# Kernel optimization log

Measured on AMD Instinct MI355X. Metric: run time of the kernel, lower is better.

The kernel has to match this reference:

```python
import jax, jax.numpy as jnp
import numpy as np

CLAMP = 10.0  # forward default arg `clamp`


def setup_inputs() -> dict:
    key = jax.random.key(0)
    k1, k2, k3, k4 = jax.random.split(key, 4)
    B, N = 256, 8192
    return {
        "pred_frames": jax.random.normal(k1, (B, N, 4, 4), dtype=jnp.float32),
        "true_frames": jax.random.normal(k2, (B, N, 4, 4), dtype=jnp.float32),
        "pred_pos": jax.random.normal(k3, (B, N, 3), dtype=jnp.float32),
        "true_pos": jax.random.normal(k4, (B, N, 3), dtype=jnp.float32),
    }


def reference(pred_frames, true_frames, pred_pos, true_pos):
    # Batched Kabsch alignment of pred_pos -> true_pos, then clamped point error.
    # pred_frames / true_frames are unused by the original module's forward.
    cA = pred_pos.mean(axis=1, keepdims=True)  # [B,1,3]
    cB = true_pos.mean(axis=1, keepdims=True)  # [B,1,3]
    AA = pred_pos - cA                          # [B,N,3]
    BB = true_pos - cB                          # [B,N,3]
    H = jnp.einsum('bni,bnj->bij', AA, BB)      # [B,3,3] covariance
    U, S, Vt = jnp.linalg.svd(H)
    # R = Vt^T @ U^T : R[b,i,k] = sum_j Vt[b,j,i] * U[b,k,j]
    R = jnp.einsum('bji,bkj->bik', Vt, U)
    det = jnp.linalg.det(R)                     # [B]
    sign = jnp.where(det < 0, -1.0, 1.0).astype(Vt.dtype)
    Vt_fixed = Vt.at[:, -1, :].multiply(sign[:, None])  # flip last row if det<0
    R = jnp.einsum('bji,bkj->bik', Vt_fixed, U)
    # t = centroid_B - R @ centroid_A (vector of shape [B,3])
    t = cB[:, 0, :] - jnp.einsum('bij,bj->bi', R, cA[:, 0, :])
    # NOTE: original applies pred_pos @ R (not R^T) + t, replicated faithfully.
    pred_aligned = jnp.einsum('bni,bij->bnj', pred_pos, R) + t[:, None, :]
    dist = jnp.linalg.norm(pred_aligned - true_pos, axis=-1)  # [B,N]
    # clamp(max=CLAMP).mean() per batch, then averaged over batch == global mean
    return jnp.mean(jnp.minimum(dist, CLAMP))
```

## Files before the change

### kernel.cpp

```cpp
#include <hip/hip_runtime.h>
#include <math.h>

#define NB 256
#define NPT 8192
#define SPLITS 4
#define CHUNK (NPT / SPLITS)
#define THREADS 256
#define CLAMPV 10.0f
#define INV_TOTAL (1.0f / 2097152.0f)

__global__ __launch_bounds__(THREADS) void cov_kernel(
    const float* __restrict__ pred, const float* __restrict__ tru,
    float* __restrict__ stats)
{
    const int blk = blockIdx.x;
    const int b  = blk >> 2;
    const int sp = blk & 3;
    const float* P = pred + ((size_t)b * NPT + (size_t)sp * CHUNK) * 3;
    const float* T = tru  + ((size_t)b * NPT + (size_t)sp * CHUNK) * 3;

    float acc[15];
#pragma unroll
    for (int i = 0; i < 15; ++i) acc[i] = 0.f;

    for (int n0 = threadIdx.x * 4; n0 < CHUNK; n0 += THREADS * 4) {
        const float4* Pq = (const float4*)(P + 3 * n0);
        const float4* Tq = (const float4*)(T + 3 * n0);
        const float4 pa = Pq[0], pb = Pq[1], pc = Pq[2];
        const float4 ta = Tq[0], tb = Tq[1], tc = Tq[2];
        const float px[4] = {pa.x, pa.w, pb.z, pc.y};
        const float py[4] = {pa.y, pb.x, pb.w, pc.z};
        const float pz[4] = {pa.z, pb.y, pc.x, pc.w};
        const float tx[4] = {ta.x, ta.w, tb.z, tc.y};
        const float ty[4] = {ta.y, tb.x, tb.w, tc.z};
        const float tz[4] = {ta.z, tb.y, tc.x, tc.w};
#pragma unroll
        for (int k = 0; k < 4; ++k) {
            acc[0] += px[k]; acc[1] += py[k]; acc[2] += pz[k];
            acc[3] += tx[k]; acc[4] += ty[k]; acc[5] += tz[k];
            acc[6]  += px[k]*tx[k]; acc[7]  += px[k]*ty[k]; acc[8]  += px[k]*tz[k];
            acc[9]  += py[k]*tx[k]; acc[10] += py[k]*ty[k]; acc[11] += py[k]*tz[k];
            acc[12] += pz[k]*tx[k]; acc[13] += pz[k]*ty[k]; acc[14] += pz[k]*tz[k];
        }
    }
#pragma unroll
    for (int i = 0; i < 15; ++i)
        for (int off = 32; off > 0; off >>= 1)
            acc[i] += __shfl_down(acc[i], off, 64);

    __shared__ float smem[THREADS/64][15];
    const int wave = threadIdx.x >> 6, lane = threadIdx.x & 63;
    if (lane == 0) {
#pragma unroll
        for (int i = 0; i < 15; ++i) smem[wave][i] = acc[i];
    }
    __syncthreads();
    if (threadIdx.x < 15) {
        float s = 0.f;
#pragma unroll
        for (int w = 0; w < THREADS/64; ++w) s += smem[w][threadIdx.x];
        stats[(size_t)blk * 16 + threadIdx.x] = s;
    }
}

__device__ inline double det3(const double m[3][3]) {
    return m[0][0]*(m[1][1]*m[2][2]-m[1][2]*m[2][1])
         - m[0][1]*(m[1][0]*m[2][2]-m[1][2]*m[2][0])
         + m[0][2]*(m[1][0]*m[2][1]-m[1][1]*m[2][0]);
}

__global__ void svd_kernel(const float* __restrict__ stats, float* __restrict__ RT,
                           float* __restrict__ out)
{
    const int b = blockIdx.x * blockDim.x + threadIdx.x;
    if (b == 0) out[0] = 0.f;
    if (b >= NB) return;

    double sA[3] = {0,0,0}, sB[3] = {0,0,0}, M[9] = {0,0,0,0,0,0,0,0,0};
    for (int sp = 0; sp < SPLITS; ++sp) {
        const float* st = stats + ((size_t)(b * SPLITS + sp)) * 16;
        for (int i = 0; i < 3; ++i) sA[i] += st[i];
        for (int i = 0; i < 3; ++i) sB[i] += st[3 + i];
        for (int i = 0; i < 9; ++i) M[i]  += st[6 + i];
    }
    double cA[3], cB[3];
    for (int i = 0; i < 3; ++i) { cA[i] = sA[i] / NPT; cB[i] = sB[i] / NPT; }

    double H[3][3];
    for (int i = 0; i < 3; ++i)
        for (int j = 0; j < 3; ++j)
            H[i][j] = M[i*3 + j] - (double)NPT * cA[i] * cB[j];

    double A[3][3];
    for (int i = 0; i < 3; ++i)
        for (int j = 0; j < 3; ++j) {
            double s = 0.0;
            for (int k = 0; k < 3; ++k) s += H[k][i] * H[k][j];
            A[i][j] = s;
        }
    double V[3][3] = {{1,0,0},{0,1,0},{0,0,1}};
    const int PQ[3][2] = {{0,1},{0,2},{1,2}};
    for (int sweep = 0; sweep < 6; ++sweep) {
        for (int r = 0; r < 3; ++r) {
            const int p = PQ[r][0], q = PQ[r][1];
            const double apq = A[p][q];
            if (fabs(apq) < 1e-300) continue;
            const double theta = (A[q][q] - A[p][p]) / (2.0 * apq);
            const double t = copysign(1.0, theta) / (fabs(theta) + sqrt(theta*theta + 1.0));
            const double c = 1.0 / sqrt(t*t + 1.0);
            const double s = t * c;
            for (int k = 0; k < 3; ++k) {
                const double akp = A[k][p], akq = A[k][q];
                A[k][p] = c*akp - s*akq;
                A[k][q] = s*akp + c*akq;
            }
            for (int k = 0; k < 3; ++k) {
                const double apk = A[p][k], aqk = A[q][k];
                A[p][k] = c*apk - s*aqk;
                A[q][k] = s*apk + c*aqk;
            }
            for (int k = 0; k < 3; ++k) {
                const double vkp = V[k][p], vkq = V[k][q];
                V[k][p] = c*vkp - s*vkq;
                V[k][q] = s*vkp + c*vkq;
            }
        }
    }
    double eig[3] = {A[0][0], A[1][1], A[2][2]};
    int idx[3] = {0, 1, 2};
    if (eig[idx[0]] < eig[idx[1]]) { int t_ = idx[0]; idx[0] = idx[1]; idx[1] = t_; }
    if (eig[idx[0]] < eig[idx[2]]) { int t_ = idx[0]; idx[0] = idx[2]; idx[2] = t_; }
    if (eig[idx[1]] < eig[idx[2]]) { int t_ = idx[1]; idx[1] = idx[2]; idx[2] = t_; }

    double Vc[3][3], Uc[3][3];
    for (int i = 0; i < 3; ++i) {
        const int j = idx[i];
        for (int r = 0; r < 3; ++r) Vc[r][i] = V[r][j];
    }
    for (int i = 0; i < 3; ++i) {
        double u[3];
        for (int r = 0; r < 3; ++r)
            u[r] = H[r][0]*Vc[0][i] + H[r][1]*Vc[1][i] + H[r][2]*Vc[2][i];
        const double nrm = sqrt(u[0]*u[0] + u[1]*u[1] + u[2]*u[2]);
        if (nrm > 1e-30) {
            for (int r = 0; r < 3; ++r) Uc[r][i] = u[r] / nrm;
        } else if (i == 2) {
            Uc[0][2] = Uc[1][0]*Uc[2][1] - Uc[2][0]*Uc[1][1];
            Uc[1][2] = Uc[2][0]*Uc[0][1] - Uc[0][0]*Uc[2][1];
            Uc[2][2] = Uc[0][0]*Uc[1][1] - Uc[1][0]*Uc[0][1];
        } else {
            for (int r = 0; r < 3; ++r) Uc[r][i] = (r == i) ? 1.0 : 0.0;
        }
    }
    if (det3(Uc) * det3(Vc) < 0.0)
        for (int r = 0; r < 3; ++r) Vc[r][2] = -Vc[r][2];

    double R[3][3];
    for (int i = 0; i < 3; ++i)
        for (int k = 0; k < 3; ++k)
            R[i][k] = Vc[i][0]*Uc[k][0] + Vc[i][1]*Uc[k][1] + Vc[i][2]*Uc[k][2];
    double tv[3];
    for (int i = 0; i < 3; ++i)
        tv[i] = cB[i] - (R[i][0]*cA[0] + R[i][1]*cA[1] + R[i][2]*cA[2]);

    float* o = RT + (size_t)b * 12;
    for (int i = 0; i < 3; ++i)
        for (int j = 0; j < 3; ++j)
            o[i*3 + j] = (float)R[i][j];
    for (int i = 0; i < 3; ++i) o[9 + i] = (float)tv[i];
}

__global__ __launch_bounds__(THREADS) void dist_kernel(
    const float* __restrict__ pred, const float* __restrict__ tru,
    const float* __restrict__ RT, float* __restrict__ out)
{
    const int blk = blockIdx.x;
    const int b  = blk >> 2;
    const int sp = blk & 3;
    const float* P = pred + ((size_t)b * NPT + (size_t)sp * CHUNK) * 3;
    const float* T = tru  + ((size_t)b * NPT + (size_t)sp * CHUNK) * 3;
    const float* rt = RT + (size_t)b * 12;
    const float R00 = rt[0], R01 = rt[1], R02 = rt[2];
    const float R10 = rt[3], R11 = rt[4], R12 = rt[5];
    const float R20 = rt[6], R21 = rt[7], R22 = rt[8];
    const float t0 = rt[9], t1 = rt[10], t2 = rt[11];

    float acc = 0.f;
    for (int n0 = threadIdx.x * 4; n0 < CHUNK; n0 += THREADS * 4) {
        const float4* Pq = (const float4*)(P + 3 * n0);
        const float4* Tq = (const float4*)(T + 3 * n0);
        const float4 pa = Pq[0], pb = Pq[1], pc = Pq[2];
        const float4 ta = Tq[0], tb = Tq[1], tc = Tq[2];
        const float px[4] = {pa.x, pa.w, pb.z, pc.y};
        const float py[4] = {pa.y, pb.x, pb.w, pc.z};
        const float pz[4] = {pa.z, pb.y, pc.x, pc.w};
        const float tx[4] = {ta.x, ta.w, tb.z, tc.y};
        const float ty[4] = {ta.y, tb.x, tb.w, tc.z};
        const float tz[4] = {ta.z, tb.y, tc.x, tc.w};
#pragma unroll
        for (int k = 0; k < 4; ++k) {
            const float ax = px[k]*R00 + py[k]*R10 + pz[k]*R20 + t0;
            const float ay = px[k]*R01 + py[k]*R11 + pz[k]*R21 + t1;
            const float az = px[k]*R02 + py[k]*R12 + pz[k]*R22 + t2;
            const float dx = ax - tx[k], dy = ay - ty[k], dz = az - tz[k];
            const float d = sqrtf(dx*dx + dy*dy + dz*dz);
            acc += fminf(d, CLAMPV);
        }
    }
    for (int off = 32; off > 0; off >>= 1)
        acc += __shfl_down(acc, off, 64);
    __shared__ float smem[THREADS/64];
    const int wave = threadIdx.x >> 6, lane = threadIdx.x & 63;
    if (lane == 0) smem[wave] = acc;
    __syncthreads();
    if (threadIdx.x == 0) {
        float s = 0.f;
#pragma unroll
        for (int w = 0; w < THREADS/64; ++w) s += smem[w];
        atomicAdd(out, s * INV_TOTAL);
    }
}

extern "C" void kernel_launch(void* const* d_in, const int* in_sizes, int n_in,
                              void* d_out, int out_size, void* d_ws, size_t ws_size,
                              hipStream_t stream)
{
    const float* pred_pos = (const float*)d_in[2];
    const float* true_pos = (const float*)d_in[3];
    float* out = (float*)d_out;

    float* ws    = (float*)d_ws;
    float* stats = ws;
    float* RT    = ws + (size_t)NB * SPLITS * 16;

    cov_kernel<<<NB * SPLITS, THREADS, 0, stream>>>(pred_pos, true_pos, stats);
    svd_kernel<<<1, NB, 0, stream>>>(stats, RT, out);
    dist_kernel<<<NB * SPLITS, THREADS, 0, stream>>>(pred_pos, true_pos, RT, out);
}
```

Baseline: 276.0 us.

## Use float one-sided Jacobi SVD and spread the SVD kernel over more blocks

Replaces the double-precision eigen-decomposition of H^T H with a single-precision one-sided Jacobi iteration that rotates H's columns directly, so singular values and U come out of the rotated columns. The SVD kernel is also launched as four 64-thread blocks instead of one 256-thread block. The goal is to shorten the serial small-matrix stage between the two streaming kernels, at the cost of reduced precision in the covariance and rotation, which could matter for near-degenerate H.

New measurement: 273.5 us. Within noise of the previous version (-0.9%).

```diff
diff --git a/kernel.cpp b/kernel.cpp
--- a/kernel.cpp
+++ b/kernel.cpp
@@ -63,111 +63,99 @@
     }
 }
 
-__device__ inline double det3(const double m[3][3]) {
+__device__ inline float det3f(const float m[3][3]) {
     return m[0][0]*(m[1][1]*m[2][2]-m[1][2]*m[2][1])
          - m[0][1]*(m[1][0]*m[2][2]-m[1][2]*m[2][0])
          + m[0][2]*(m[1][0]*m[2][1]-m[1][1]*m[2][0]);
 }
 
-__global__ void svd_kernel(const float* __restrict__ stats, float* __restrict__ RT,
-                           float* __restrict__ out)
-{
-    const int b = blockIdx.x * blockDim.x + threadIdx.x;
+__global__ __launch_bounds__(64) void svd_kernel(
+    const float* __restrict__ stats, float* __restrict__ RT,
+    float* __restrict__ out)
+{
+    const int b = blockIdx.x * 64 + threadIdx.x;
     if (b == 0) out[0] = 0.f;
     if (b >= NB) return;
 
-    double sA[3] = {0,0,0}, sB[3] = {0,0,0}, M[9] = {0,0,0,0,0,0,0,0,0};
+    float sA[3] = {0,0,0}, sB[3] = {0,0,0}, M[9] = {0,0,0,0,0,0,0,0,0};
     for (int sp = 0; sp < SPLITS; ++sp) {
         const float* st = stats + ((size_t)(b * SPLITS + sp)) * 16;
         for (int i = 0; i < 3; ++i) sA[i] += st[i];
         for (int i = 0; i < 3; ++i) sB[i] += st[3 + i];
         for (int i = 0; i < 9; ++i) M[i]  += st[6 + i];
     }
-    double cA[3], cB[3];
-    for (int i = 0; i < 3; ++i) { cA[i] = sA[i] / NPT; cB[i] = sB[i] / NPT; }
-
-    double H[3][3];
+    float cA[3], cB[3];
+    for (int i = 0; i < 3; ++i) { cA[i] = sA[i] * (1.f/NPT); cB[i] = sB[i] * (1.f/NPT); }
+
+    float W[3][3], V[3][3] = {{1,0,0},{0,1,0},{0,0,1}};
     for (int i = 0; i < 3; ++i)
         for (int j = 0; j < 3; ++j)
-            H[i][j] = M[i*3 + j] - (double)NPT * cA[i] * cB[j];
-
-    double A[3][3];
-    for (int i = 0; i < 3; ++i)
-        for (int j = 0; j < 3; ++j) {
-            double s = 0.0;
-            for (int k = 0; k < 3; ++k) s += H[k][i] * H[k][j];
-            A[i][j] = s;
-        }
-    double V[3][3] = {{1,0,0},{0,1,0},{0,0,1}};
+            W[i][j] = M[i*3 + j] - (float)NPT * cA[i] * cB[j];
+
     const int PQ[3][2] = {{0,1},{0,2},{1,2}};
-    for (int sweep = 0; sweep < 6; ++sweep) {
+    for (int sweep = 0; sweep < 8; ++sweep) {
         for (int r = 0; r < 3; ++r) {
             const int p = PQ[r][0], q = PQ[r][1];
-            const double apq = A[p][q];
-            if (fabs(apq) < 1e-300) continue;
-            const double theta = (A[q][q] - A[p][p]) / (2.0 * apq);
-            const double t = copysign(1.0, theta) / (fabs(theta) + sqrt(theta*theta + 1.0));
-            const double c = 1.0 / sqrt(t*t + 1.0);
-            const double s = t * c;
+            const float app = W[0][p]*W[0][p] + W[1][p]*W[1][p] + W[2][p]*W[2][p];
+            const float aqq = W[0][q]*W[0][q] + W[1][q]*W[1][q] + W[2][q]*W[2][q];
+            const float apq = W[0][p]*W[0][q] + W[1][p]*W[1][q] + W[2][p]*W[2][q];
+            if (fabsf(apq) < 1e-30f) continue;
+            const float theta = (aqq - app) / (2.f * apq);
+            const float t = copysignf(1.f, theta) / (fabsf(theta) + sqrtf(theta*theta + 1.f));
+            const float c = 1.f / sqrtf(t*t + 1.f);
+            const float s = t * c;
+#pragma unroll
             for (int k = 0; k < 3; ++k) {
-                const double akp = A[k][p], akq = A[k][q];
-                A[k][p] = c*akp - s*akq;
-                A[k][q] = s*akp + c*akq;
-            }
-            for (int k = 0; k < 3; ++k) {
-                const double apk = A[p][k], aqk = A[q][k];
-                A[p][k] = c*apk - s*aqk;
-                A[q][k] = s*apk + c*aqk;
-            }
-            for (int k = 0; k < 3; ++k) {
-                const double vkp = V[k][p], vkq = V[k][q];
+                const float wkp = W[k][p], wkq = W[k][q];
+                W[k][p] = c*wkp - s*wkq;
+                W[k][q] = s*wkp + c*wkq;
+                const float vkp = V[k][p], vkq = V[k][q];
                 V[k][p] = c*vkp - s*vkq;
                 V[k][q] = s*vkp + c*vkq;
             }
         }
     }
-    double eig[3] = {A[0][0], A[1][1], A[2][2]};
+    float sig[3];
+    for (int c = 0; c < 3; ++c)
+        sig[c] = sqrtf(W[0][c]*W[0][c] + W[1][c]*W[1][c] + W[2][c]*W[2][c]);
+
     int idx[3] = {0, 1, 2};
-    if (eig[idx[0]] < eig[idx[1]]) { int t_ = idx[0]; idx[0] = idx[1]; idx[1] = t_; }
-    if (eig[idx[0]] < eig[idx[2]]) { int t_ = idx[0]; idx[0] = idx[2]; idx[2] = t_; }
-    if (eig[idx[1]] < eig[idx[2]]) { int t_ = idx[1]; idx[1] = idx[2]; idx[2] = t_; }
-
-    double Vc[3][3], Uc[3][3];
+    if (sig[idx[0]] < sig[idx[1]]) { int t_ = idx[0]; idx[0] = idx[1]; idx[1] = t_; }
+    if (sig[idx[0]] < sig[idx[2]]) { int t_ = idx[0]; idx[0] = idx[2]; idx[2] = t_; }
+    if (sig[idx[1]] < sig[idx[2]]) { int t_ = idx[1]; idx[1] = idx[2]; idx[2] = t_; }
+
+    float Vc[3][3], Uc[3][3];
     for (int i = 0; i < 3; ++i) {
         const int j = idx[i];
         for (int r = 0; r < 3; ++r) Vc[r][i] = V[r][j];
-    }
-    for (int i = 0; i < 3; ++i) {
-        double u[3];
-        for (int r = 0; r < 3; ++r)
-            u[r] = H[r][0]*Vc[0][i] + H[r][1]*Vc[1][i] + H[r][2]*Vc[2][i];
-        const double nrm = sqrt(u[0]*u[0] + u[1]*u[1] + u[2]*u[2]);
-        if (nrm > 1e-30) {
-            for (int r = 0; r < 3; ++r) Uc[r][i] = u[r] / nrm;
+        const float sg = sig[j];
+        if (sg > 1e-20f) {
+            const float inv = 1.f / sg;
+            for (int r = 0; r < 3; ++r) Uc[r][i] = W[r][j] * inv;
         } else if (i == 2) {
             Uc[0][2] = Uc[1][0]*Uc[2][1] - Uc[2][0]*Uc[1][1];
             Uc[1][2] = Uc[2][0]*Uc[0][1] - Uc[0][0]*Uc[2][1];
             Uc[2][2] = Uc[0][0]*Uc[1][1] - Uc[1][0]*Uc[0][1];
         } else {
-            for (int r = 0; r < 3; ++r) Uc[r][i] = (r == i) ? 1.0 : 0.0;
-        }
-    }
-    if (det3(Uc) * det3(Vc) < 0.0)
+            for (int r = 0; r < 3; ++r) Uc[r][i] = (r == i) ? 1.f : 0.f;
+        }
+    }
+    if (det3f(Uc) * det3f(Vc) < 0.f)
         for (int r = 0; r < 3; ++r) Vc[r][2] = -Vc[r][2];
 
-    double R[3][3];
+    float R[3][3];
     for (int i = 0; i < 3; ++i)
         for (int k = 0; k < 3; ++k)
             R[i][k] = Vc[i][0]*Uc[k][0] + Vc[i][1]*Uc[k][1] + Vc[i][2]*Uc[k][2];
-    double tv[3];
+    float tv[3];
     for (int i = 0; i < 3; ++i)
         tv[i] = cB[i] - (R[i][0]*cA[0] + R[i][1]*cA[1] + R[i][2]*cA[2]);
 
     float* o = RT + (size_t)b * 12;
     for (int i = 0; i < 3; ++i)
         for (int j = 0; j < 3; ++j)
-            o[i*3 + j] = (float)R[i][j];
-    for (int i = 0; i < 3; ++i) o[9 + i] = (float)tv[i];
+            o[i*3 + j] = R[i][j];
+    for (int i = 0; i < 3; ++i) o[9 + i] = tv[i];
 }
 
 __global__ __launch_bounds__(THREADS) void dist_kernel(
@@ -234,6 +222,6 @@
     float* RT    = ws + (size_t)NB * SPLITS * 16;
 
     cov_kernel<<<NB * SPLITS, THREADS, 0, stream>>>(pred_pos, true_pos, stats);
-    svd_kernel<<<1, NB, 0, stream>>>(stats, RT, out);
+    svd_kernel<<<NB / 64, 64, 0, stream>>>(stats, RT, out);
     dist_kernel<<<NB * SPLITS, THREADS, 0, stream>>>(pred_pos, true_pos, RT, out);
 }
```
